# Performance work log

Hardware: AMD Instinct MI355X
Metric: run time of the kernel (lower is better)

Reference implementation:

```python
import jax, jax.numpy as jnp
import numpy as np

D = 128
NQ = 25  # r2d2 quantized AP: 25 triangular bins over similarity range [0, 1]


def grid_sample_bilinear(img, grid):
    """F.grid_sample, mode='bilinear', padding_mode='zeros', align_corners=False.
    img: (B,C,H,W), grid: (B,Hg,Wg,2) in [-1,1] (x, y order). -> (B,C,Hg,Wg)"""
    B, C, H, W = img.shape
    gx = ((grid[..., 0] + 1.0) * W - 1.0) * 0.5  # (B,Hg,Wg) unnormalized x
    gy = ((grid[..., 1] + 1.0) * H - 1.0) * 0.5
    x0f = jnp.floor(gx)
    y0f = jnp.floor(gy)
    wx1 = gx - x0f
    wy1 = gy - y0f
    x0 = x0f.astype(jnp.int32)
    y0 = y0f.astype(jnp.int32)

    def gather(yi, xi):
        valid = ((xi >= 0) & (xi < W) & (yi >= 0) & (yi < H)).astype(img.dtype)
        xc = jnp.clip(xi, 0, W - 1)
        yc = jnp.clip(yi, 0, H - 1)
        v = jax.vmap(lambda im, y, x: im[:, y, x])(img, yc, xc)  # (B,C,Hg,Wg)
        return v * valid[:, None]

    out = (gather(y0, x0) * ((1 - wy1) * (1 - wx1))[:, None]
           + gather(y0, x0 + 1) * ((1 - wy1) * wx1)[:, None]
           + gather(y0 + 1, x0) * (wy1 * (1 - wx1))[:, None]
           + gather(y0 + 1, x0 + 1) * (wy1 * wx1)[:, None])
    return out


def quantized_ap(sim, lab):
    """r2d2 QAPLoss: soft-histogram differentiable AP.
    sim: (B,N,M) similarities, lab: (B,N,M) binary labels (float). -> (B,N) AP per query."""
    a = jnp.float32(NQ - 1)                 # slope; bin width = 1/a over gap [0,1]
    c = jnp.linspace(1.0, 0.0, NQ, dtype=sim.dtype)  # bin centers, descending score
    # triangular kernel membership: relu(1 - a*|s - c|), shape (B,N,Q,M)
    q = jnp.maximum(0.0, 1.0 - a * jnp.abs(sim[:, :, None, :] - c[None, None, :, None]))
    nbs = q.sum(-1)                          # (B,N,Q) soft count per bin
    rec = (q * lab[:, :, None, :]).sum(-1)   # (B,N,Q) soft positive count per bin
    prec = jnp.cumsum(rec, -1) / (1e-16 + jnp.cumsum(nbs, -1))
    rec = rec / rec.sum(-1, keepdims=True)
    return (prec * rec).sum(-1)              # (B,N)


def setup_inputs() -> dict:
    key = jax.random.key(0)
    k1, k2, k3, k4, k5 = jax.random.split(key, 5)
    B, H, W = 2, 32, 32
    d1 = jax.random.normal(k1, (B, D, H, W), dtype=jnp.float32)
    d2 = jax.random.normal(k2, (B, D, H, W), dtype=jnp.float32)
    # L2-normalize over channels (r2d2 descriptors are unit-norm -> sims in [-1,1])
    d1 = d1 / jnp.linalg.norm(d1, axis=1, keepdims=True)
    d2 = d2 / jnp.linalg.norm(d2, axis=1, keepdims=True)
    rel = jax.random.uniform(k3, (B, 1, H, W), dtype=jnp.float32)
    grid = jax.random.uniform(k4, (B, H, W, 2), dtype=jnp.float32) * 1.8 - 0.9  # in [-0.9,0.9]
    label = jax.random.randint(k5, (B, H, W, H, W), 0, 2, dtype=jnp.int32)
    return {"desc1": d1, "desc2": d2, "reliability": rel, "grid": grid, "label": label}


def reference(desc1, desc2, reliability, grid, label):
    B, C, H, W = desc1.shape
    d2w = grid_sample_bilinear(desc2, grid)           # warp image2 descriptors
    q = desc1.reshape(B, C, H * W).transpose(0, 2, 1)  # (B,N,C)
    db = d2w.reshape(B, C, H * W).transpose(0, 2, 1)   # (B,M,C)
    sim = jnp.einsum('bnd,bmd->bnm', q, db)            # per-sample pairwise similarity
    lab = label.reshape(B, H * W, H * W).astype(sim.dtype)
    ap = quantized_ap(sim, lab)                        # (B,N)
    return jnp.mean(ap)                                # mAP over queries and batch
```

## Files before the change

### kernel.cpp

```cpp
#include <hip/hip_runtime.h>


#define NQB 25

template<int CTRL>
__device__ __forceinline__ float dppadd(float v) {
    int s = __builtin_amdgcn_update_dpp(0, __float_as_int(v), CTRL, 0xf, 0xf, true);
    return v + __int_as_float(s);
}
__device__ __forceinline__ float red16(float v) {
    v = dppadd<0xB1>(v);
    v = dppadd<0x4E>(v);
    v = dppadd<0x141>(v);
    v = dppadd<0x140>(v);
    return v;
}

__global__ __launch_bounds__(256) void k_gs(const float* __restrict__ desc2,
                                            const float* __restrict__ grd,
                                            float* __restrict__ dbt)
{
    __shared__ float plane[1024];
    int r = blockIdx.x;
    int b = r >> 7;
    int tid = threadIdx.x;
    const float* src = desc2 + ((size_t)r << 10);
    *(float4*)&plane[tid * 4] = *(const float4*)&src[tid * 4];
    __syncthreads();
#pragma unroll
    for (int e = 0; e < 4; e++) {
        int m = tid + (e << 8);
        int pos = (b << 10) + m;
        float2 g = ((const float2*)grd)[pos];
        float fx = ((g.x + 1.f) * 32.f - 1.f) * 0.5f;
        float fy = ((g.y + 1.f) * 32.f - 1.f) * 0.5f;
        float x0f = floorf(fx), y0f = floorf(fy);
        float wx1 = fx - x0f, wy1 = fy - y0f;
        float wx0 = 1.f - wx1, wy0 = 1.f - wy1;
        int x0 = (int)x0f, y0 = (int)y0f;
        float acc = 0.f;
        if ((unsigned)y0 < 32u && (unsigned)x0 < 32u)
            acc += wy0 * wx0 * plane[(y0 << 5) + x0];
        if ((unsigned)y0 < 32u && (unsigned)(x0 + 1) < 32u)
            acc += wy0 * wx1 * plane[(y0 << 5) + x0 + 1];
        if ((unsigned)(y0 + 1) < 32u && (unsigned)x0 < 32u)
            acc += wy1 * wx0 * plane[((y0 + 1) << 5) + x0];
        if ((unsigned)(y0 + 1) < 32u && (unsigned)(x0 + 1) < 32u)
            acc += wy1 * wx1 * plane[((y0 + 1) << 5) + x0 + 1];
        dbt[((size_t)r << 10) + m] = acc;
    }
}

__device__ __forceinline__ void loadc(const float* __restrict__ dp, int ch,
                                      float* d)
{
    int cb = ch << 3;
#pragma unroll
    for (int i = 0; i < 8; i++) {
        d[i]     = dp[(size_t)(cb + i) << 10];
        d[8 + i] = dp[(((size_t)(cb + i)) << 10) + 512];
    }
}
__device__ __forceinline__ void fmac(const float* __restrict__ d1, int ch,
                                     const float* d, float* a0, float* a1)
{
    int cb = ch << 3;
#pragma unroll
    for (int i = 0; i < 8; i++) {
        const float* qp = d1 + ((size_t)(cb + i) << 10);
#pragma unroll
        for (int qq = 0; qq < 8; qq++) {
            float qv = qp[qq];
            a0[qq] = fmaf(qv, d[i], a0[qq]);
            a1[qq] = fmaf(qv, d[8 + i], a1[qq]);
        }
    }
}

__global__ __launch_bounds__(512) void k_main(const float* __restrict__ desc1,
                                              const float* __restrict__ dbt,
                                              const int* __restrict__ label,
                                              float* __restrict__ appart)
{
    __shared__ float s[8][1024];
    __shared__ float CNs[8][4][NQB];
    __shared__ float CRs[8][4][NQB];
    __shared__ float apb[8];

    int tid = threadIdx.x;
    int qg0 = blockIdx.x << 3;
    int b = qg0 >> 10;
    int n0 = qg0 & 1023;

    int q = tid >> 6, l = tid & 63;
    const int* lp = label + ((size_t)(qg0 + q) << 10) + l;
    int lv[16];
#pragma unroll
    for (int e = 0; e < 16; e++) lv[e] = lp[(size_t)(e << 6)];

    const float* d1 = desc1 + ((size_t)b << 17) + n0;
    const float* dp = dbt + ((size_t)b << 17) + tid;

    float a0[8], a1[8];
#pragma unroll
    for (int qq = 0; qq < 8; qq++) { a0[qq] = 0.f; a1[qq] = 0.f; }

    float dA[16], dB[16];
    loadc(dp, 0, dA);
    for (int ch = 0; ch < 16; ch += 2) {
        loadc(dp, ch + 1, dB);
        fmac(d1, ch, dA, a0, a1);
        if (ch + 2 < 16) loadc(dp, ch + 2, dA);
        fmac(d1, ch + 1, dB, a0, a1);
    }
#pragma unroll
    for (int qq = 0; qq < 8; qq++) { s[qq][tid] = a0[qq]; s[qq][tid + 512] = a1[qq]; }
    __syncthreads();

    float CN[NQB], CR[NQB];
#pragma unroll
    for (int k = 0; k < NQB; k++) { CN[k] = 0.f; CR[k] = 0.f; }
#pragma unroll
    for (int e = 0; e < 16; e++) {
        float sv = s[q][l + (e << 6)];
        float lfv = (float)lv[e];
        float u = fmaf(-24.f, sv, 24.f);
#pragma unroll
        for (int k = 0; k < NQB; k++) {
            float t = fminf(fmaxf((float)(k + 1) - u, 0.f), 1.f);
            CN[k] += t;
            CR[k] = fmaf(lfv, t, CR[k]);
        }
    }
#pragma unroll
    for (int k = 0; k < NQB; k++) { CN[k] = red16(CN[k]); CR[k] = red16(CR[k]); }
    if ((l & 15) == 0) {
        int rec = l >> 4;
#pragma unroll
        for (int k = 0; k < NQB; k++) { CNs[q][rec][k] = CN[k]; CRs[q][rec][k] = CR[k]; }
    }
    __syncthreads();

    if (tid < 8) {
        float ap = 0.f, prev = 0.f;
#pragma unroll
        for (int k = 0; k < NQB; k++) {
            float cn = CNs[tid][0][k] + CNs[tid][1][k] + CNs[tid][2][k] + CNs[tid][3][k];
            float cr = CRs[tid][0][k] + CRs[tid][1][k] + CRs[tid][2][k] + CRs[tid][3][k];
            float pr = cr / (1e-16f + cn);
            ap += pr * (cr - prev);
            prev = cr;
        }
        apb[tid] = ap / prev;
    }
    __syncthreads();
    if (tid == 0) {
        float v = 0.f;
#pragma unroll
        for (int q2 = 0; q2 < 8; q2++) v += apb[q2];
        appart[blockIdx.x] = v;
    }
}

__global__ __launch_bounds__(256) void k_final(const float* __restrict__ appart,
                                               float* __restrict__ out,
                                               int nb, float invn)
{
    int tid = threadIdx.x;
    float v = 0.f;
    for (int i = tid; i < nb; i += 256) v += appart[i];
    for (int off = 32; off; off >>= 1) v += __shfl_xor(v, off, 64);
    __shared__ float wsum[4];
    if ((tid & 63) == 0) wsum[tid >> 6] = v;
    __syncthreads();
    if (tid == 0) out[0] = (wsum[0] + wsum[1] + wsum[2] + wsum[3]) * invn;
}

extern "C" void kernel_launch(void* const* d_in, const int* in_sizes, int n_in,
                              void* d_out, int out_size, void* d_ws, size_t ws_size,
                              hipStream_t stream)
{
    const float* desc1 = (const float*)d_in[0];
    const float* desc2 = (const float*)d_in[1];
    const float* grd   = (const float*)d_in[3];
    const int*   label = (const int*)d_in[4];

    int B = in_sizes[0] / (128 * 1024);
    int npos = B * 1024;

    float* ws = (float*)d_ws;
    float* dbt    = ws;
    float* appart = dbt + (size_t)npos * 128;
    float* out = (float*)d_out;

    k_gs<<<B * 128, 256, 0, stream>>>(desc2, grd, dbt);
    k_main<<<npos / 8, 512, 0, stream>>>(desc1, dbt, label, appart);
    k_final<<<1, 256, 0, stream>>>(appart, out, npos / 8, 1.f / (float)npos);
}
```

Before: 27.89 us.

## Split fused similarity+histogram kernel into separate tiled GEMM and histogram kernels

The fused kernel, where each block computed 8 query rows against all 1024 database columns before histogramming, is split into a separate 64x64-tiled GEMM kernel that writes the full similarity matrix to workspace, followed by a histogram kernel that reads it back. The tiled GEMM gives more blocks and more output reuse per loaded database value. The cost is an extra kernel launch and an 8 MB round trip of similarity values through global memory.

```diff
diff --git a/kernel.cpp b/kernel.cpp
--- a/kernel.cpp
+++ b/kernel.cpp
@@ -51,80 +51,81 @@
     }
 }
 
-__device__ __forceinline__ void loadc(const float* __restrict__ dp, int ch,
-                                      float* d)
-{
-    int cb = ch << 3;
-#pragma unroll
-    for (int i = 0; i < 8; i++) {
-        d[i]     = dp[(size_t)(cb + i) << 10];
-        d[8 + i] = dp[(((size_t)(cb + i)) << 10) + 512];
-    }
-}
-__device__ __forceinline__ void fmac(const float* __restrict__ d1, int ch,
-                                     const float* d, float* a0, float* a1)
-{
-    int cb = ch << 3;
-#pragma unroll
-    for (int i = 0; i < 8; i++) {
-        const float* qp = d1 + ((size_t)(cb + i) << 10);
-#pragma unroll
-        for (int qq = 0; qq < 8; qq++) {
-            float qv = qp[qq];
-            a0[qq] = fmaf(qv, d[i], a0[qq]);
-            a1[qq] = fmaf(qv, d[8 + i], a1[qq]);
-        }
-    }
-}
-
-__global__ __launch_bounds__(512) void k_main(const float* __restrict__ desc1,
+__global__ __launch_bounds__(256) void k_gemm(const float* __restrict__ desc1,
                                               const float* __restrict__ dbt,
+                                              float* __restrict__ simm)
+{
+    int bid = blockIdx.x;
+    int b = bid >> 8;
+    int r = bid & 255;
+    int qt = r >> 4, mt = r & 15;
+    int tid = threadIdx.x;
+    int ty = tid >> 6, lane = tid & 63;
+
+    const float* d1 = desc1 + ((size_t)b << 17) + qt * 64 + ty * 16;
+    const float* dp = dbt + ((size_t)b << 17) + mt * 64 + lane;
+
+    float acc[16];
+#pragma unroll
+    for (int j = 0; j < 16; j++) acc[j] = 0.f;
+
+    float dA[8], dB[8];
+#define LOADC(buf, ch) { int cb = (ch) << 3;                                   \
+    _Pragma("unroll")                                                          \
+    for (int i = 0; i < 8; i++) buf[i] = dp[(size_t)(cb + i) << 10]; }
+#define FMAC(ch, buf) { int cb = (ch) << 3;                                    \
+    _Pragma("unroll")                                                          \
+    for (int i = 0; i < 8; i++) {                                              \
+        const float* qp = d1 + ((size_t)(cb + i) << 10);                       \
+        _Pragma("unroll")                                                      \
+        for (int j = 0; j < 16; j++) acc[j] = fmaf(qp[j], buf[i], acc[j]); } }
+
+    LOADC(dA, 0);
+    for (int ch = 0; ch < 16; ch += 2) {
+        LOADC(dB, ch + 1);
+        FMAC(ch, dA);
+        if (ch + 2 < 16) LOADC(dA, ch + 2);
+        FMAC(ch + 1, dB);
+    }
+#undef LOADC
+#undef FMAC
+
+    float* sp = simm + ((((size_t)(b << 10)) + qt * 64 + ty * 16) << 10)
+              + mt * 64 + lane;
+#pragma unroll
+    for (int j = 0; j < 16; j++) sp[(size_t)j << 10] = acc[j];
+}
+
+__global__ __launch_bounds__(512) void k_hist(const float* __restrict__ simm,
                                               const int* __restrict__ label,
                                               float* __restrict__ appart)
 {
-    __shared__ float s[8][1024];
     __shared__ float CNs[8][4][NQB];
     __shared__ float CRs[8][4][NQB];
     __shared__ float apb[8];
 
     int tid = threadIdx.x;
     int qg0 = blockIdx.x << 3;
-    int b = qg0 >> 10;
-    int n0 = qg0 & 1023;
-
     int q = tid >> 6, l = tid & 63;
-    const int* lp = label + ((size_t)(qg0 + q) << 10) + l;
+    int qg = qg0 + q;
+
+    const int* lp = label + ((size_t)qg << 10) + l;
+    const float* sp = simm + ((size_t)qg << 10) + l;
+
     int lv[16];
+    float sv[16];
 #pragma unroll
     for (int e = 0; e < 16; e++) lv[e] = lp[(size_t)(e << 6)];
-
-    const float* d1 = desc1 + ((size_t)b << 17) + n0;
-    const float* dp = dbt + ((size_t)b << 17) + tid;
-
-    float a0[8], a1[8];
-#pragma unroll
-    for (int qq = 0; qq < 8; qq++) { a0[qq] = 0.f; a1[qq] = 0.f; }
-
-    float dA[16], dB[16];
-    loadc(dp, 0, dA);
-    for (int ch = 0; ch < 16; ch += 2) {
-        loadc(dp, ch + 1, dB);
-        fmac(d1, ch, dA, a0, a1);
-        if (ch + 2 < 16) loadc(dp, ch + 2, dA);
-        fmac(d1, ch + 1, dB, a0, a1);
-    }
-#pragma unroll
-    for (int qq = 0; qq < 8; qq++) { s[qq][tid] = a0[qq]; s[qq][tid + 512] = a1[qq]; }
-    __syncthreads();
+#pragma unroll
+    for (int e = 0; e < 16; e++) sv[e] = sp[(size_t)(e << 6)];
 
     float CN[NQB], CR[NQB];
 #pragma unroll
     for (int k = 0; k < NQB; k++) { CN[k] = 0.f; CR[k] = 0.f; }
 #pragma unroll
     for (int e = 0; e < 16; e++) {
-        float sv = s[q][l + (e << 6)];
+        float u = fmaf(-24.f, sv[e], 24.f);
         float lfv = (float)lv[e];
-        float u = fmaf(-24.f, sv, 24.f);
 #pragma unroll
         for (int k = 0; k < NQB; k++) {
             float t = fminf(fmaxf((float)(k + 1) - u, 0.f), 1.f);
@@ -162,9 +163,9 @@
     }
 }
 
-__global__ __launch_bounds__(256) void k_final(const float* __restrict__ appart,
-                                               float* __restrict__ out,
-                                               int nb, float invn)
+__global__ __launch_bounds__(256) void k_sum(const float* __restrict__ appart,
+                                             float* __restrict__ out,
+                                             int nb, float invn)
 {
     int tid = threadIdx.x;
     float v = 0.f;
@@ -190,10 +191,12 @@
 
     float* ws = (float*)d_ws;
     float* dbt    = ws;
-    float* appart = dbt + (size_t)npos * 128;
+    float* simm   = dbt + (size_t)npos * 128;
+    float* appart = simm + (size_t)npos * 1024;
     float* out = (float*)d_out;
 
     k_gs<<<B * 128, 256, 0, stream>>>(desc2, grd, dbt);
-    k_main<<<npos / 8, 512, 0, stream>>>(desc1, dbt, label, appart);
-    k_final<<<1, 256, 0, stream>>>(appart, out, npos / 8, 1.f / (float)npos);
-}
+    k_gemm<<<B * 256, 256, 0, stream>>>(desc1, dbt, simm);
+    k_hist<<<npos / 8, 512, 0, stream>>>(simm, label, appart);
+    k_sum<<<1, 256, 0, stream>>>(appart, out, npos / 8, 1.f / (float)npos);
+}
```

New measurement: 55.87 us. +100.3%, slower.

## Fold bilinear warp into similarity by interpolating dot products instead of descriptors

Applied to the files above, without the earlier changes.

Removes the separate grid-sample kernel and uses the linearity of bilinear interpolation. Each block now takes dot products of its queries against the unwarped desc2 positions, stores them in shared memory, and then bilinearly interpolates the similarity row at each grid location using the four neighbour weights. This drops a kernel launch and the round trip of the warped descriptor buffer through global memory. In exchange each thread does four shared-memory gathers and some extra ALU per element, and the result changes slightly from floating-point reassociation.

```diff
diff --git a/kernel.cpp b/kernel.cpp
--- a/kernel.cpp
+++ b/kernel.cpp
@@ -14,41 +14,6 @@
     v = dppadd<0x141>(v);
     v = dppadd<0x140>(v);
     return v;
-}
-
-__global__ __launch_bounds__(256) void k_gs(const float* __restrict__ desc2,
-                                            const float* __restrict__ grd,
-                                            float* __restrict__ dbt)
-{
-    __shared__ float plane[1024];
-    int r = blockIdx.x;
-    int b = r >> 7;
-    int tid = threadIdx.x;
-    const float* src = desc2 + ((size_t)r << 10);
-    *(float4*)&plane[tid * 4] = *(const float4*)&src[tid * 4];
-    __syncthreads();
-#pragma unroll
-    for (int e = 0; e < 4; e++) {
-        int m = tid + (e << 8);
-        int pos = (b << 10) + m;
-        float2 g = ((const float2*)grd)[pos];
-        float fx = ((g.x + 1.f) * 32.f - 1.f) * 0.5f;
-        float fy = ((g.y + 1.f) * 32.f - 1.f) * 0.5f;
-        float x0f = floorf(fx), y0f = floorf(fy);
-        float wx1 = fx - x0f, wy1 = fy - y0f;
-        float wx0 = 1.f - wx1, wy0 = 1.f - wy1;
-        int x0 = (int)x0f, y0 = (int)y0f;
-        float acc = 0.f;
-        if ((unsigned)y0 < 32u && (unsigned)x0 < 32u)
-            acc += wy0 * wx0 * plane[(y0 << 5) + x0];
-        if ((unsigned)y0 < 32u && (unsigned)(x0 + 1) < 32u)
-            acc += wy0 * wx1 * plane[(y0 << 5) + x0 + 1];
-        if ((unsigned)(y0 + 1) < 32u && (unsigned)x0 < 32u)
-            acc += wy1 * wx0 * plane[((y0 + 1) << 5) + x0];
-        if ((unsigned)(y0 + 1) < 32u && (unsigned)(x0 + 1) < 32u)
-            acc += wy1 * wx1 * plane[((y0 + 1) << 5) + x0 + 1];
-        dbt[((size_t)r << 10) + m] = acc;
-    }
 }
 
 __device__ __forceinline__ void loadc(const float* __restrict__ dp, int ch,
@@ -78,7 +43,8 @@
 }
 
 __global__ __launch_bounds__(512) void k_main(const float* __restrict__ desc1,
-                                              const float* __restrict__ dbt,
+                                              const float* __restrict__ desc2,
+                                              const float* __restrict__ grd,
                                               const int* __restrict__ label,
                                               float* __restrict__ appart)
 {
@@ -97,9 +63,13 @@
     int lv[16];
 #pragma unroll
     for (int e = 0; e < 16; e++) lv[e] = lp[(size_t)(e << 6)];
+    const float2* gp = (const float2*)grd + ((size_t)b << 10) + l;
+    float2 gv[16];
+#pragma unroll
+    for (int e = 0; e < 16; e++) gv[e] = gp[(size_t)(e << 6)];
 
     const float* d1 = desc1 + ((size_t)b << 17) + n0;
-    const float* dp = dbt + ((size_t)b << 17) + tid;
+    const float* dp = desc2 + ((size_t)b << 17) + tid;
 
     float a0[8], a1[8];
 #pragma unroll
@@ -120,11 +90,32 @@
     float CN[NQB], CR[NQB];
 #pragma unroll
     for (int k = 0; k < NQB; k++) { CN[k] = 0.f; CR[k] = 0.f; }
+    const float* sq = s[q];
 #pragma unroll
     for (int e = 0; e < 16; e++) {
-        float sv = s[q][l + (e << 6)];
+        float gx = gv[e].x, gy = gv[e].y;
+        float fx = ((gx + 1.f) * 32.f - 1.f) * 0.5f;
+        float fy = ((gy + 1.f) * 32.f - 1.f) * 0.5f;
+        float x0f = floorf(fx), y0f = floorf(fy);
+        float wx1 = fx - x0f, wy1 = fy - y0f;
+        float wx0 = 1.f - wx1, wy0 = 1.f - wy1;
+        int x0 = (int)x0f, y0 = (int)y0f;
+        int x1 = x0 + 1, y1 = y0 + 1;
+        bool bx0 = (unsigned)x0 < 32u, bx1 = (unsigned)x1 < 32u;
+        bool by0 = (unsigned)y0 < 32u, by1 = (unsigned)y1 < 32u;
+        float w00 = (by0 && bx0) ? wy0 * wx0 : 0.f;
+        float w01 = (by0 && bx1) ? wy0 * wx1 : 0.f;
+        float w10 = (by1 && bx0) ? wy1 * wx0 : 0.f;
+        float w11 = (by1 && bx1) ? wy1 * wx1 : 0.f;
+        int xc0 = min(max(x0, 0), 31), xc1 = min(max(x1, 0), 31);
+        int yc0 = min(max(y0, 0), 31), yc1 = min(max(y1, 0), 31);
+        float sv = w00 * sq[(yc0 << 5) + xc0];
+        sv = fmaf(w01, sq[(yc0 << 5) + xc1], sv);
+        sv = fmaf(w10, sq[(yc1 << 5) + xc0], sv);
+        sv = fmaf(w11, sq[(yc1 << 5) + xc1], sv);
+
+        float u = fmaf(-24.f, sv, 24.f);
         float lfv = (float)lv[e];
-        float u = fmaf(-24.f, sv, 24.f);
 #pragma unroll
         for (int k = 0; k < NQB; k++) {
             float t = fminf(fmaxf((float)(k + 1) - u, 0.f), 1.f);
@@ -187,13 +178,12 @@
 
     int B = in_sizes[0] / (128 * 1024);
     int npos = B * 1024;
+    int nblk = npos / 8;
 
     float* ws = (float*)d_ws;
-    float* dbt    = ws;
-    float* appart = dbt + (size_t)npos * 128;
+    float* appart = ws;
     float* out = (float*)d_out;
 
-    k_gs<<<B * 128, 256, 0, stream>>>(desc2, grd, dbt);
-    k_main<<<npos / 8, 512, 0, stream>>>(desc1, dbt, label, appart);
-    k_final<<<1, 256, 0, stream>>>(appart, out, npos / 8, 1.f / (float)npos);
+    k_main<<<nblk, 512, 0, stream>>>(desc1, desc2, grd, label, appart);
+    k_final<<<1, 256, 0, stream>>>(appart, out, nblk, 1.f / (float)npos);
 }
```

Result: faster. 25.63 us, median of 3 (-8.1%).
